# Optimization experiments

Measured on AMD Instinct MI355X. Metric: run time of the kernel, lower is better.

Reference implementation:

```python
import jax, jax.numpy as jnp
import numpy as np

N = 2000  # nodes per graph (hardcoded in the original module)


def gatv2(x, src, dst, edge_attr, Wl, Wr, We, att, b):
    """PyG GATv2Conv (concat=True, negative_slope=0.2, edge_dim) forward.
    x: [N, Fin]; src/dst: [E]; edge_attr: [E, 2]; att: [H, C]. Returns [N, H*C]."""
    n = x.shape[0]
    H, C = att.shape
    xl = (x @ Wl).reshape(n, H, C)            # messages from source nodes
    xr = (x @ Wr).reshape(n, H, C)            # target-node term
    ee = (edge_attr @ We).reshape(-1, H, C)   # edge feature term
    m = jax.nn.leaky_relu(xl[src] + xr[dst] + ee, 0.2)
    logits = jnp.einsum('ehc,hc->eh', m, att)           # [E, H]
    lmax = jax.ops.segment_max(logits, dst, num_segments=n)
    p = jnp.exp(logits - lmax[dst])
    denom = jax.ops.segment_sum(p, dst, num_segments=n)
    alpha = p / (denom[dst] + 1e-16)                    # scatter-softmax over in-edges
    out = jax.ops.segment_sum(alpha[:, :, None] * xl[src], dst, num_segments=n)
    return out.reshape(n, H * C) + b


def setup_inputs() -> dict:
    key = jax.random.key(0)
    ks = jax.random.split(key, 32)
    B, T, F, E = 4, 10, 8, 16000
    s = 0.05
    d = {
        'x': jax.random.normal(ks[0], (B, T, N, F), jnp.float32),
        'edge_index': jax.random.randint(ks[1], (2, E), 0, N, jnp.int32),
        'edge_attr': jax.random.normal(ks[2], (E, 2), jnp.float32),
        'w_l0': s * jax.random.normal(ks[3], (8, 128)),
        'w_r0': s * jax.random.normal(ks[4], (8, 128)),
        'w_e0': s * jax.random.normal(ks[5], (2, 128)),
        'att0': s * jax.random.normal(ks[6], (4, 32)),
        'b0': s * jax.random.normal(ks[7], (128,)),
        'w_l1': s * jax.random.normal(ks[8], (128, 128)),
        'w_r1': s * jax.random.normal(ks[9], (128, 128)),
        'w_e1': s * jax.random.normal(ks[10], (2, 128)),
        'att1': s * jax.random.normal(ks[11], (4, 32)),
        'b1': s * jax.random.normal(ks[12], (128,)),
        'w_l2': s * jax.random.normal(ks[13], (128, 32)),
        'w_r2': s * jax.random.normal(ks[14], (128, 32)),
        'w_e2': s * jax.random.normal(ks[15], (2, 32)),
        'att2': s * jax.random.normal(ks[16], (4, 8)),
        'b2': s * jax.random.normal(ks[17], (32,)),
        'w_ih': s * jax.random.normal(ks[18], (1024, 64000)),
        'w_hh': s * jax.random.normal(ks[19], (1024, 256)),
        'b_ih': s * jax.random.normal(ks[20], (1024,)),
        'b_hh': s * jax.random.normal(ks[21], (1024,)),
        'fc1_w': s * jax.random.normal(ks[22], (256, 512)),
        'fc1_b': s * jax.random.normal(ks[23], (512,)),
        'fc2_w': s * jax.random.normal(ks[24], (512, 1)),
        'fc2_b': s * jax.random.normal(ks[25], (1,)),
    }
    return d


def reference(x, edge_index, edge_attr, w_l0, w_r0, w_e0, att0, b0,
              w_l1, w_r1, w_e1, att1, b1, w_l2, w_r2, w_e2, att2, b2,
              w_ih, w_hh, b_ih, b_hh, fc1_w, fc1_b, fc2_w, fc2_b):
    B, T = x.shape[0], x.shape[1]
    # PyG GATv2Conv add_self_loops=True with fill_value='mean' for edge_attr
    loop = jnp.arange(N, dtype=edge_index.dtype)
    src = jnp.concatenate([edge_index[0], loop])
    dst = jnp.concatenate([edge_index[1], loop])
    ea = jnp.concatenate([edge_attr, jnp.broadcast_to(edge_attr.mean(0), (N, 2))], axis=0)

    def gat_stack(xt):  # [N, F] -> [N*32] flattened embedding
        h = jax.nn.relu(gatv2(xt, src, dst, ea, w_l0, w_r0, w_e0, att0, b0))
        h = jax.nn.relu(gatv2(h, src, dst, ea, w_l1, w_r1, w_e1, att1, b1))
        h = jax.nn.relu(gatv2(h, src, dst, ea, w_l2, w_r2, w_e2, att2, b2))
        return h.reshape(-1)

    emb = jax.vmap(jax.vmap(gat_stack))(x)  # [B, T, 64000]

    # single-layer LSTM (torch gate order: i, f, g, o)
    Hh = w_hh.shape[1]
    def step(carry, xt):
        h, c = carry
        g = xt @ w_ih.T + h @ w_hh.T + (b_ih + b_hh)
        i, f, gg, o = jnp.split(g, 4, axis=-1)
        c = jax.nn.sigmoid(f) * c + jax.nn.sigmoid(i) * jnp.tanh(gg)
        h = jax.nn.sigmoid(o) * jnp.tanh(c)
        return (h, c), h
    h0 = jnp.zeros((B, Hh), emb.dtype)
    (_, _), hs = jax.lax.scan(step, (h0, h0), jnp.swapaxes(emb, 0, 1))  # hs: [T, B, Hh]

    last = jax.nn.relu(hs[-1])                       # relu(lstm_out)[:, -1, :]
    hid = jax.nn.relu(last @ fc1_w + fc1_b)          # (dropout=0 -> identity)
    return hid @ fc2_w + fc2_b                       # [B, 1]
```

## Files before the change

### kernel.cpp

```cpp
#include <hip/hip_runtime.h>
#include <hip/hip_bf16.h>
#include <math.h>

typedef __hip_bfloat16 bf16;
typedef __attribute__((ext_vector_type(8))) short short8;
typedef __attribute__((ext_vector_type(4))) float f32x4;

#define NNODES 2000
#define NEDGE_IN 16000
#define NEDGE 18000
#define NGRAPH 40
#define GATES_KS 80

__device__ __forceinline__ float bf2f(bf16 v){ return __bfloat162float(v); }
__device__ __forceinline__ bf16 f2bf(float v){ return __float2bfloat16(v); }
__device__ __forceinline__ short bfbits(float v){ bf16 t = __float2bfloat16(v); return *reinterpret_cast<short*>(&t); }
__device__ __forceinline__ float blo(unsigned u){ return __uint_as_float(u<<16); }
__device__ __forceinline__ float bhi(unsigned u){ return __uint_as_float(u & 0xffff0000u); }

__global__ __launch_bounds__(256) void k_setup(const float* __restrict__ ea, float* __restrict__ mean_ea,
                        const float* __restrict__ whh, unsigned* __restrict__ whhT2,
                        const float* __restrict__ w1a, const float* __restrict__ w1b,
                        const float* __restrict__ w2a, const float* __restrict__ w2b,
                        bf16* __restrict__ b1a, bf16* __restrict__ b1b,
                        bf16* __restrict__ b2a, bf16* __restrict__ b2b,
                        int* __restrict__ cnt, int* __restrict__ cursor,
                        const float* __restrict__ X, const float* __restrict__ Wa,
                        const float* __restrict__ Wb,
                        bf16* __restrict__ Ya, bf16* __restrict__ Yb){
  __shared__ float smem[2048];
  int bb = blockIdx.x, tid = threadIdx.x;
  if (bb >= 689){
    int blk = bb - 689;
    for (int i = tid; i < 1024; i += 256){ smem[i] = Wa[i]; smem[1024+i] = Wb[i]; }
    __syncthreads();
    int j  = tid & 127;
    int rg = tid >> 7;
    size_t m0 = (size_t)blk*8 + (size_t)rg*4;
    const float* x0 = X + m0*8;
    float a0=0.f,a1=0.f,a2=0.f,a3=0.f, b0=0.f,b1=0.f,b2=0.f,b3=0.f;
    #pragma unroll
    for (int k=0;k<8;k++){
      float wa = smem[k*128 + j], wb = smem[1024 + k*128 + j];
      float x_0 = x0[k], x_1 = x0[8+k], x_2 = x0[16+k], x_3 = x0[24+k];
      a0 += x_0*wa; a1 += x_1*wa; a2 += x_2*wa; a3 += x_3*wa;
      b0 += x_0*wb; b1 += x_1*wb; b2 += x_2*wb; b3 += x_3*wb;
    }
    bf16* ya = Ya + m0*128 + j;
    bf16* yb = Yb + m0*128 + j;
    ya[0]=f2bf(a0); ya[128]=f2bf(a1); ya[256]=f2bf(a2); ya[384]=f2bf(a3);
    yb[0]=f2bf(b0); yb[128]=f2bf(b1); yb[256]=f2bf(b2); yb[384]=f2bf(b3);
  } else if (bb == 0){
    float* s0l = smem; float* s1l = smem + 256;
    float s0=0.f, s1=0.f;
    for (int e = tid; e < NEDGE_IN; e += 256){ s0 += ea[2*e]; s1 += ea[2*e+1]; }
    s0l[tid]=s0; s1l[tid]=s1; __syncthreads();
    for (int d=128; d>=1; d>>=1){
      if (tid < d){ s0l[tid]+=s0l[tid+d]; s1l[tid]+=s1l[tid+d]; }
      __syncthreads();
    }
    if (tid==0){ mean_ea[0]=s0l[0]/(float)NEDGE_IN; mean_ea[1]=s1l[0]/(float)NEDGE_IN; }
  } else if (bb < 513){
    int idx = (bb-1)*256 + tid;
    int j = idx >> 7, kp = idx & 127;
    unsigned ulo = (unsigned)(unsigned short)bfbits(whh[j*256 + 2*kp]);
    unsigned uhi = (unsigned)(unsigned short)bfbits(whh[j*256 + 2*kp + 1]);
    whhT2[kp*1024 + j] = (uhi<<16) | ulo;
  } else if (bb < 673){
    int idx = (bb-513)*256 + tid;
    const float* src; bf16* dst; int n, local;
    if (idx < 16384){ src=w1a; dst=b1a; n=128; local=idx; }
    else if (idx < 32768){ src=w1b; dst=b1b; n=128; local=idx-16384; }
    else if (idx < 36864){ src=w2a; dst=b2a; n=32; local=idx-32768; }
    else { src=w2b; dst=b2b; n=32; local=idx-36864; }
    int k = local / n, c = local % n;
    dst[c*128 + k] = f2bf(src[local]);
  } else {
    int idx = (bb-673)*256 + tid;
    if (idx < 2000) cnt[idx] = 0;
    else if (idx < 4000) cursor[idx-2000] = 0;
  }
}

__global__ void k_count(const int* __restrict__ ei, int* __restrict__ cnt){
  int e = blockIdx.x*256 + threadIdx.x;
  if (e >= NEDGE) return;
  int d = (e < NEDGE_IN) ? ei[NEDGE_IN + e] : (e - NEDGE_IN);
  atomicAdd(&cnt[d], 1);
}

__global__ void k_scan(const int* __restrict__ cnt, int* __restrict__ off){
  __shared__ int s[2048];
  int lane = threadIdx.x;
  for (int i = lane; i < 2048; i += 64) s[i] = (i < NNODES) ? cnt[i] : 0;
  __syncthreads();
  int base = lane*32, run = 0;
  for (int j=0;j<32;j++){ int t = s[base+j]; s[base+j] = run; run += t; }
  int x = run;
  for (int d=1; d<64; d<<=1){ int y = __shfl_up(x, d); if (lane >= d) x += y; }
  int chunkOff = x - run;
  for (int j=0;j<32;j++){ int idx = base+j; if (idx <= NNODES) off[idx] = chunkOff + s[idx]; }
}

__global__ void k_scatter(const int* __restrict__ ei, const int* __restrict__ off,
                          int* __restrict__ cursor, const float* __restrict__ ea,
                          const float* __restrict__ mean_ea,
                          int* __restrict__ csr_src, float2* __restrict__ eaP){
  int e = blockIdx.x*256 + threadIdx.x;
  if (e >= NEDGE) return;
  int d, sn; float2 a;
  if (e < NEDGE_IN){ sn = ei[e]; d = ei[NEDGE_IN+e]; a = ((const float2*)ea)[e]; }
  else { sn = e-NEDGE_IN; d = sn; a.x = mean_ea[0]; a.y = mean_ea[1]; }
  int p = off[d] + atomicAdd(&cursor[d], 1);
  csr_src[p] = sn;
  eaP[p] = a;
}

template<int N>
__global__ __launch_bounds__(256) void k_gemm_mf2(const bf16* __restrict__ A, const bf16* __restrict__ BTa,
                                                  const bf16* __restrict__ BTb,
                                                  bf16* __restrict__ Ya, bf16* __restrict__ Yb){
  const int NT = N/16;
  int lane = threadIdx.x & 63, wv = threadIdx.x >> 6;
  size_t m0 = (size_t)blockIdx.x*128 + (size_t)wv*32;
  int r = lane & 15, kg = lane >> 4;
  const f32x4 zero = {0.f,0.f,0.f,0.f};
  f32x4 acca[2][NT], accb[2][NT];
  #pragma unroll
  for (int s=0;s<2;s++)
    #pragma unroll
    for (int t=0;t<NT;t++){ acca[s][t] = zero; accb[s][t] = zero; }
  #pragma unroll
  for (int c=0;c<4;c++){
    short8 a0 = *(const short8*)(A + (m0 + r)*128 + c*32 + kg*8);
    short8 a1 = *(const short8*)(A + (m0 + 16 + r)*128 + c*32 + kg*8);
    #pragma unroll
    for (int t=0;t<NT;t++){
      short8 ba = *(const short8*)(BTa + (size_t)(t*16 + r)*128 + c*32 + kg*8);
      short8 bb = *(const short8*)(BTb + (size_t)(t*16 + r)*128 + c*32 + kg*8);
      acca[0][t] = __builtin_amdgcn_mfma_f32_16x16x32_bf16(a0, ba, acca[0][t], 0,0,0);
      acca[1][t] = __builtin_amdgcn_mfma_f32_16x16x32_bf16(a1, ba, acca[1][t], 0,0,0);
      accb[0][t] = __builtin_amdgcn_mfma_f32_16x16x32_bf16(a0, bb, accb[0][t], 0,0,0);
      accb[1][t] = __builtin_amdgcn_mfma_f32_16x16x32_bf16(a1, bb, accb[1][t], 0,0,0);
    }
  }
  #pragma unroll
  for (int s=0;s<2;s++)
    #pragma unroll
    for (int t=0;t<NT;t++){
      size_t row = m0 + s*16 + kg*4;
      int col = t*16 + r;
      #pragma unroll
      for (int i=0;i<4;i++){
        Ya[(row+i)*N + col] = f2bf(acca[s][t][i]);
        Yb[(row+i)*N + col] = f2bf(accb[s][t][i]);
      }
    }
}

__global__ __launch_bounds__(256) void k_edge_g(const bf16* __restrict__ XL, const bf16* __restrict__ XR,
                                                const float2* __restrict__ eaP, const int* __restrict__ off,
                                                const int* __restrict__ csr_src, const float* __restrict__ att,
                                                const float* __restrict__ We, const float* __restrict__ bias,
                                                bf16* __restrict__ Hout){
  int tid = threadIdx.x;
  int ln = tid & 63;
  int gq = tid >> 6;
  int n  = blockIdx.x;
  int c0 = 2*ln;
  float av0 = att[c0], av1 = att[c0+1];
  float w00 = We[c0], w01 = We[c0+1];
  float w10 = We[128+c0], w11 = We[128+c0+1];
  const unsigned* XLu = (const unsigned*)XL;
  const unsigned* XRu = (const unsigned*)XR;
  float xr0[10], xr1[10], srun[10], acc0[10], acc1[10];
  #pragma unroll
  for (int t=0;t<10;t++){
    int g = gq*10 + t;
    unsigned xu = XRu[((size_t)g*NNODES + n)*64 + ln];
    xr0[t] = blo(xu); xr1[t] = bhi(xu);
    srun[t]=0.f; acc0[t]=0.f; acc1[t]=0.f;
  }
  int p0 = off[n], p1 = off[n+1];
  for (int p = p0; p < p1; ++p){
    int u = csr_src[p];
    float2 e = eaP[p];
    float ed0 = fmaf(e.x, w00, e.y*w10);
    float ed1 = fmaf(e.x, w01, e.y*w11);
    unsigned xl[10];
    #pragma unroll
    for (int t=0;t<10;t++){
      int g = gq*10 + t;
      xl[t] = XLu[((size_t)g*NNODES + u)*64 + ln];
    }
    #pragma unroll
    for (int t=0;t<10;t++){
      float x0 = blo(xl[t]), x1 = bhi(xl[t]);
      float s0 = x0 + xr0[t] + ed0;
      float s1 = x1 + xr1[t] + ed1;
      float m0 = fmaxf(s0, 0.2f*s0);
      float m1 = fmaxf(s1, 0.2f*s1);
      float c = fmaf(m0, av0, m1*av1);
      #pragma unroll
      for (int d=8; d>=1; d>>=1) c += __shfl_xor(c, d);
      float pe = __expf(c);
      srun[t] += pe;
      acc0[t] = fmaf(pe, x0, acc0[t]);
      acc1[t] = fmaf(pe, x1, acc1[t]);
    }
  }
  #pragma unroll
  for (int t=0;t<10;t++){
    int g = gq*10 + t;
    float inv = 1.f/(srun[t] + 1e-16f);
    float o0 = fmaf(acc0[t], inv, bias[c0]);
    float o1 = fmaf(acc1[t], inv, bias[c0+1]);
    o0 = fmaxf(o0, 0.f); o1 = fmaxf(o1, 0.f);
    unsigned r0 = (unsigned)(unsigned short)bfbits(o0);
    unsigned r1 = (unsigned)(unsigned short)bfbits(o1);
    ((unsigned*)Hout)[((size_t)g*NNODES + n)*64 + ln] = (r1<<16) | r0;
  }
}

template<int H, int C>
__global__ __launch_bounds__(256) void k_edge(const bf16* __restrict__ XL, const bf16* __restrict__ XR,
                                              const float2* __restrict__ eaP, const int* __restrict__ off,
                                              const int* __restrict__ csr_src, const float* __restrict__ att,
                                              const float* __restrict__ We, const float* __restrict__ bias,
                                              bf16* __restrict__ Hout){
  const int HC = H*C;
  const int LPN = HC/2;
  const int NPW = 64/LPN;
  const int NPB = 4*NPW;
  int tid = threadIdx.x;
  int lane = tid & 63, wv = tid >> 6;
  int ln = lane % LPN;
  int n  = blockIdx.x*NPB + wv*NPW + lane/LPN;
  int g  = blockIdx.y;
  int c0 = 2*ln;
  size_t gbase = (size_t)g*NNODES*HC;
  const unsigned* XLu = (const unsigned*)(XL + gbase);
  unsigned xru = ((const unsigned*)(XR + gbase))[n*LPN + ln];
  float xr0 = blo(xru), xr1 = bhi(xru);
  float av0 = att[c0], av1 = att[c0+1];
  float w00 = We[c0], w01 = We[c0+1];
  float w10 = We[HC+c0], w11 = We[HC+c0+1];
  float srun = 0.f, acc0 = 0.f, acc1 = 0.f;
  int p0 = off[n], p1 = off[n+1];
  int p = p0;
  for (; p+2 <= p1; p += 2){
    int uA = csr_src[p], uB = csr_src[p+1];
    float2 eA = eaP[p], eB = eaP[p+1];
    unsigned xlA = XLu[uA*LPN + ln];
    unsigned xlB = XLu[uB*LPN + ln];
    float xa0 = blo(xlA), xa1 = bhi(xlA);
    float xb0 = blo(xlB), xb1 = bhi(xlB);
    float sa0 = xa0 + fmaf(eA.x,w00, fmaf(eA.y,w10, xr0));
    float sa1 = xa1 + fmaf(eA.x,w01, fmaf(eA.y,w11, xr1));
    float sb0 = xb0 + fmaf(eB.x,w00, fmaf(eB.y,w10, xr0));
    float sb1 = xb1 + fmaf(eB.x,w01, fmaf(eB.y,w11, xr1));
    float ma0 = fmaxf(sa0, 0.2f*sa0), ma1 = fmaxf(sa1, 0.2f*sa1);
    float mb0 = fmaxf(sb0, 0.2f*sb0), mb1 = fmaxf(sb1, 0.2f*sb1);
    float cA = fmaf(ma0,av0, ma1*av1);
    float cB = fmaf(mb0,av0, mb1*av1);
    #pragma unroll
    for (int d=C/4; d>=1; d>>=1){ cA += __shfl_xor(cA, d); cB += __shfl_xor(cB, d); }
    float peA = __expf(cA), peB = __expf(cB);
    srun += peA + peB;
    acc0 = fmaf(peA, xa0, fmaf(peB, xb0, acc0));
    acc1 = fmaf(peA, xa1, fmaf(peB, xb1, acc1));
  }
  if (p < p1){
    int uA = csr_src[p];
    float2 eA = eaP[p];
    unsigned xlA = XLu[uA*LPN + ln];
    float xa0 = blo(xlA), xa1 = bhi(xlA);
    float sa0 = xa0 + fmaf(eA.x,w00, fmaf(eA.y,w10, xr0));
    float sa1 = xa1 + fmaf(eA.x,w01, fmaf(eA.y,w11, xr1));
    float ma0 = fmaxf(sa0, 0.2f*sa0), ma1 = fmaxf(sa1, 0.2f*sa1);
    float cA = fmaf(ma0,av0, ma1*av1);
    #pragma unroll
    for (int d=C/4; d>=1; d>>=1) cA += __shfl_xor(cA, d);
    float peA = __expf(cA);
    srun += peA;
    acc0 = fmaf(peA, xa0, acc0);
    acc1 = fmaf(peA, xa1, acc1);
  }
  float inv = 1.f/(srun + 1e-16f);
  float o0 = fmaf(acc0, inv, bias[c0]);
  float o1 = fmaf(acc1, inv, bias[c0+1]);
  o0 = fmaxf(o0, 0.f); o1 = fmaxf(o1, 0.f);
  unsigned r0 = (unsigned)(unsigned short)bfbits(o0);
  unsigned r1 = (unsigned)(unsigned short)bfbits(o1);
  ((unsigned*)(Hout + gbase))[n*LPN + ln] = (r1<<16) | r0;
}

__global__ __launch_bounds__(256) void k_gates_mf(const bf16* __restrict__ emb, const float* __restrict__ wih,
                                                  float* __restrict__ part){
  const int nk = 2000/GATES_KS;
  int lane = threadIdx.x & 63, wv = threadIdx.x >> 6;
  int r = lane & 15, kg = lane >> 4;
  int j0 = (blockIdx.x*4 + wv)*16;
  int ks = blockIdx.y;
  int k0 = ks*nk*32;
  const f32x4 zero = {0.f,0.f,0.f,0.f};
  f32x4 acc0 = zero, acc1 = zero, acc2 = zero;
  const float* wrow = wih + (size_t)(j0 + r)*64000;
  const bf16*  e0p  = emb + (size_t)r*64000;
  const bf16*  e1p  = emb + (size_t)(16+r)*64000;
  const bf16*  e2p  = emb + (size_t)(32+r)*64000;
  #pragma unroll 2
  for (int s=0; s<nk; ++s){
    int k = k0 + s*32 + kg*8;
    float4 wa = *(const float4*)(wrow + k);
    float4 wb = *(const float4*)(wrow + k + 4);
    short8 bfr;
    bfr[0]=bfbits(wa.x); bfr[1]=bfbits(wa.y); bfr[2]=bfbits(wa.z); bfr[3]=bfbits(wa.w);
    bfr[4]=bfbits(wb.x); bfr[5]=bfbits(wb.y); bfr[6]=bfbits(wb.z); bfr[7]=bfbits(wb.w);
    short8 a0 = *(const short8*)(e0p + k);
    short8 a1 = *(const short8*)(e1p + k);
    short8 a2 = *(const short8*)(e2p + k);
    acc0 = __builtin_amdgcn_mfma_f32_16x16x32_bf16(a0, bfr, acc0, 0,0,0);
    acc1 = __builtin_amdgcn_mfma_f32_16x16x32_bf16(a1, bfr, acc1, 0,0,0);
    acc2 = __builtin_amdgcn_mfma_f32_16x16x32_bf16(a2, bfr, acc2, 0,0,0);
  }
  int col = j0 + r;
  float* prow = part + (size_t)ks*40960;
  #pragma unroll
  for (int i=0;i<4;i++){
    int row = kg*4 + i;
    prow[(size_t)row*1024 + col] = acc0[i];
    prow[(size_t)(row+16)*1024 + col] = acc1[i];
    if (row + 32 < 40) prow[(size_t)(row+32)*1024 + col] = acc2[i];
  }
}

__global__ __launch_bounds__(256) void k_gred(const float* __restrict__ part, float* __restrict__ gates){
  int idx = blockIdx.x*256 + threadIdx.x;
  float s = 0.f;
  #pragma unroll 8
  for (int ks=0; ks<GATES_KS; ks++) s += part[(size_t)ks*40960 + idx];
  gates[idx] = s;
}

__global__ __launch_bounds__(1024) void k_lstm10h(const float* __restrict__ gates, const unsigned* __restrict__ whhT2,
                                                  const float* __restrict__ bih, const float* __restrict__ bhh,
                                                  const float* __restrict__ fc1w, const float* __restrict__ fc1b,
                                                  const float* __restrict__ fc2w, const float* __restrict__ fc2b,
                                                  float* __restrict__ out){
  __shared__ float hs[256];
  __shared__ float g[1024];
  int b = blockIdx.x, j = threadIdx.x;
  float c_reg = 0.f;
  if (j < 256) hs[j] = 0.f;
  float bias = bih[j] + bhh[j];
  __syncthreads();
  for (int t=0;t<10;t++){
    float acc = gates[(size_t)(b*10+t)*1024 + j] + bias;
    #pragma unroll 16
    for (int kp=0;kp<128;kp++){
      unsigned u = whhT2[kp*1024 + j];
      float2 h2 = *(const float2*)&hs[2*kp];
      acc = fmaf(blo(u), h2.x, acc);
      acc = fmaf(bhi(u), h2.y, acc);
    }
    g[j] = acc;
    __syncthreads();
    if (j < 256){
      float i_ = g[j], f_ = g[j+256], gg = g[j+512], o_ = g[j+768];
      float si = 1.f/(1.f+__expf(-i_));
      float sf = 1.f/(1.f+__expf(-f_));
      float so = 1.f/(1.f+__expf(-o_));
      c_reg = sf*c_reg + si*tanhf(gg);
      hs[j] = so*tanhf(c_reg);
    }
    __syncthreads();
  }
  if (j < 512){
    float acc = fc1b[j];
    for (int k=0;k<256;k++){
      float l = fmaxf(hs[k], 0.f);
      acc = fmaf(l, fc1w[k*512 + j], acc);
    }
    float hid = fmaxf(acc, 0.f);
    g[j] = hid * fc2w[j];
  }
  __syncthreads();
  for (int d=256; d>=1; d>>=1){
    if (j < d) g[j] += g[j+d];
    __syncthreads();
  }
  if (j==0) out[b] = g[0] + fc2b[0];
}

extern "C" void kernel_launch(void* const* d_in, const int* in_sizes, int n_in,
                              void* d_out, int out_size, void* d_ws, size_t ws_size,
                              hipStream_t stream){
  const float* x    = (const float*)d_in[0];
  const int*   ei   = (const int*)  d_in[1];
  const float* ea   = (const float*)d_in[2];
  const float* wl0  = (const float*)d_in[3];
  const float* wr0  = (const float*)d_in[4];
  const float* we0  = (const float*)d_in[5];
  const float* att0 = (const float*)d_in[6];
  const float* b0   = (const float*)d_in[7];
  const float* wl1  = (const float*)d_in[8];
  const float* wr1  = (const float*)d_in[9];
  const float* we1  = (const float*)d_in[10];
  const float* att1 = (const float*)d_in[11];
  const float* b1   = (const float*)d_in[12];
  const float* wl2  = (const float*)d_in[13];
  const float* wr2  = (const float*)d_in[14];
  const float* we2  = (const float*)d_in[15];
  const float* att2 = (const float*)d_in[16];
  const float* b2   = (const float*)d_in[17];
  const float* wih  = (const float*)d_in[18];
  const float* whh  = (const float*)d_in[19];
  const float* bih  = (const float*)d_in[20];
  const float* bhh  = (const float*)d_in[21];
  const float* fc1w = (const float*)d_in[22];
  const float* fc1b = (const float*)d_in[23];
  const float* fc2w = (const float*)d_in[24];
  const float* fc2b = (const float*)d_in[25];
  float* out = (float*)d_out;

  char* base = (char*)d_ws; size_t cur = 0;
  auto alloc = [&](size_t bytes)->void*{
    cur = (cur + 255) & ~(size_t)255; void* p = base + cur; cur += bytes; return p;
  };
  float* mean_ea = (float*)alloc(8);
  int*   cnt     = (int*)  alloc((size_t)NNODES*4);
  int*   off     = (int*)  alloc((size_t)(NNODES+1)*4);
  int*   cursor  = (int*)  alloc((size_t)NNODES*4);
  int*   csr_src = (int*)  alloc((size_t)NEDGE*4);
  float2* eaP    = (float2*)alloc((size_t)NEDGE*8);
  bf16*  XL      = (bf16*) alloc((size_t)80000*128*2);
  bf16*  XR      = (bf16*) alloc((size_t)80000*128*2);
  bf16*  HBUF    = (bf16*) alloc((size_t)80000*128*2);
  float* part    = (float*)alloc((size_t)GATES_KS*40960*4);
  float* gates   = (float*)alloc((size_t)40*1024*4);
  unsigned* whhT2= (unsigned*)alloc((size_t)128*1024*4);
  bf16*  bt1a    = (bf16*) alloc((size_t)128*128*2);
  bf16*  bt1b    = (bf16*) alloc((size_t)128*128*2);
  bf16*  bt2a    = (bf16*) alloc((size_t)32*128*2);
  bf16*  bt2b    = (bf16*) alloc((size_t)32*128*2);

  k_setup <<<10689,256,0,stream>>>(ea, mean_ea, whh, whhT2, wl1, wr1, wl2, wr2,
                                   bt1a, bt1b, bt2a, bt2b, cnt, cursor,
                                   x, wl0, wr0, XL, XR);
  k_count   <<<(NEDGE+255)/256,256,0,stream>>>(ei, cnt);
  k_scan    <<<1,64,0,stream>>>(cnt, off);
  k_scatter <<<(NEDGE+255)/256,256,0,stream>>>(ei, off, cursor, ea, mean_ea, csr_src, eaP);

  k_edge_g  <<<NNODES,256,0,stream>>>(XL,XR,eaP,off,csr_src,att0,we0,b0,HBUF);

  k_gemm_mf2<128> <<<625,256,0,stream>>>(HBUF, bt1a, bt1b, XL, XR);
  k_edge_g  <<<NNODES,256,0,stream>>>(XL,XR,eaP,off,csr_src,att1,we1,b1,HBUF);

  k_gemm_mf2<32> <<<625,256,0,stream>>>(HBUF, bt2a, bt2b, XL, XR);
  k_edge<4,8> <<<dim3(125,40),256,0,stream>>>(XL,XR,eaP,off,csr_src,att2,we2,b2,HBUF);

  k_gates_mf<<<dim3(16,GATES_KS),256,0,stream>>>(HBUF, wih, part);
  k_gred    <<<160,256,0,stream>>>(part, gates);

  k_lstm10h<<<4,1024,0,stream>>>(gates, whhT2, bih, bhh, fc1w, fc1b, fc2w, fc2b, out);
}
```

Baseline: 419.1 us.

## Switch node features to node-major, graph-interleaved layout for coalesced gathers

Feature buffers change from graph-major [g][n][C] to node-major [n][g][C], so gathering a source node's features for several graphs reads one contiguous region. The edge kernels, the first-layer projection and the gate GEMM's embedding indexing are all updated to match. k_edge_g is also split across two grid rows with 5 graphs per wave instead of 10, which doubles the block count and lowers per-thread register arrays. The risk is that other kernels assume the old row order: the row-wise GEMM is indifferent to it, but the LSTM gate input ordering must stay consistent.

```diff
diff --git a/kernel.cpp b/kernel.cpp
--- a/kernel.cpp
+++ b/kernel.cpp
@@ -37,6 +37,7 @@
     int j  = tid & 127;
     int rg = tid >> 7;
     size_t m0 = (size_t)blk*8 + (size_t)rg*4;
+    int g = (int)(m0/NNODES), n = (int)(m0%NNODES);
     const float* x0 = X + m0*8;
     float a0=0.f,a1=0.f,a2=0.f,a3=0.f, b0=0.f,b1=0.f,b2=0.f,b3=0.f;
     #pragma unroll
@@ -46,10 +47,11 @@
       a0 += x_0*wa; a1 += x_1*wa; a2 += x_2*wa; a3 += x_3*wa;
       b0 += x_0*wb; b1 += x_1*wb; b2 += x_2*wb; b3 += x_3*wb;
     }
-    bf16* ya = Ya + m0*128 + j;
-    bf16* yb = Yb + m0*128 + j;
-    ya[0]=f2bf(a0); ya[128]=f2bf(a1); ya[256]=f2bf(a2); ya[384]=f2bf(a3);
-    yb[0]=f2bf(b0); yb[128]=f2bf(b1); yb[256]=f2bf(b2); yb[384]=f2bf(b3);
+    const size_t RS = (size_t)NGRAPH*128;
+    bf16* ya = Ya + ((size_t)n*NGRAPH + g)*128 + j;
+    bf16* yb = Yb + ((size_t)n*NGRAPH + g)*128 + j;
+    ya[0]=f2bf(a0); ya[RS]=f2bf(a1); ya[2*RS]=f2bf(a2); ya[3*RS]=f2bf(a3);
+    yb[0]=f2bf(b0); yb[RS]=f2bf(b1); yb[2*RS]=f2bf(b2); yb[3*RS]=f2bf(b3);
   } else if (bb == 0){
     float* s0l = smem; float* s1l = smem + 256;
     float s0=0.f, s1=0.f;
@@ -167,17 +169,17 @@
   int ln = tid & 63;
   int gq = tid >> 6;
   int n  = blockIdx.x;
+  int g0 = blockIdx.y*20 + gq*5;
   int c0 = 2*ln;
   float av0 = att[c0], av1 = att[c0+1];
   float w00 = We[c0], w01 = We[c0+1];
   float w10 = We[128+c0], w11 = We[128+c0+1];
   const unsigned* XLu = (const unsigned*)XL;
   const unsigned* XRu = (const unsigned*)XR;
-  float xr0[10], xr1[10], srun[10], acc0[10], acc1[10];
-  #pragma unroll
-  for (int t=0;t<10;t++){
-    int g = gq*10 + t;
-    unsigned xu = XRu[((size_t)g*NNODES + n)*64 + ln];
+  float xr0[5], xr1[5], srun[5], acc0[5], acc1[5];
+  #pragma unroll
+  for (int t=0;t<5;t++){
+    unsigned xu = XRu[((size_t)n*NGRAPH + g0+t)*64 + ln];
     xr0[t] = blo(xu); xr1[t] = bhi(xu);
     srun[t]=0.f; acc0[t]=0.f; acc1[t]=0.f;
   }
@@ -187,14 +189,12 @@
     float2 e = eaP[p];
     float ed0 = fmaf(e.x, w00, e.y*w10);
     float ed1 = fmaf(e.x, w01, e.y*w11);
-    unsigned xl[10];
-    #pragma unroll
-    for (int t=0;t<10;t++){
-      int g = gq*10 + t;
-      xl[t] = XLu[((size_t)g*NNODES + u)*64 + ln];
-    }
-    #pragma unroll
-    for (int t=0;t<10;t++){
+    unsigned xl[5];
+    #pragma unroll
+    for (int t=0;t<5;t++)
+      xl[t] = XLu[((size_t)u*NGRAPH + g0+t)*64 + ln];
+    #pragma unroll
+    for (int t=0;t<5;t++){
       float x0 = blo(xl[t]), x1 = bhi(xl[t]);
       float s0 = x0 + xr0[t] + ed0;
       float s1 = x1 + xr1[t] + ed1;
@@ -210,15 +210,14 @@
     }
   }
   #pragma unroll
-  for (int t=0;t<10;t++){
-    int g = gq*10 + t;
+  for (int t=0;t<5;t++){
     float inv = 1.f/(srun[t] + 1e-16f);
     float o0 = fmaf(acc0[t], inv, bias[c0]);
     float o1 = fmaf(acc1[t], inv, bias[c0+1]);
     o0 = fmaxf(o0, 0.f); o1 = fmaxf(o1, 0.f);
     unsigned r0 = (unsigned)(unsigned short)bfbits(o0);
     unsigned r1 = (unsigned)(unsigned short)bfbits(o1);
-    ((unsigned*)Hout)[((size_t)g*NNODES + n)*64 + ln] = (r1<<16) | r0;
+    ((unsigned*)Hout)[((size_t)n*NGRAPH + g0+t)*64 + ln] = (r1<<16) | r0;
   }
 }
 
@@ -238,9 +237,8 @@
   int n  = blockIdx.x*NPB + wv*NPW + lane/LPN;
   int g  = blockIdx.y;
   int c0 = 2*ln;
-  size_t gbase = (size_t)g*NNODES*HC;
-  const unsigned* XLu = (const unsigned*)(XL + gbase);
-  unsigned xru = ((const unsigned*)(XR + gbase))[n*LPN + ln];
+  const unsigned* XLu = (const unsigned*)XL;
+  unsigned xru = ((const unsigned*)XR)[((size_t)n*NGRAPH + g)*LPN + ln];
   float xr0 = blo(xru), xr1 = bhi(xru);
   float av0 = att[c0], av1 = att[c0+1];
   float w00 = We[c0], w01 = We[c0+1];
@@ -251,8 +249,8 @@
   for (; p+2 <= p1; p += 2){
     int uA = csr_src[p], uB = csr_src[p+1];
     float2 eA = eaP[p], eB = eaP[p+1];
-    unsigned xlA = XLu[uA*LPN + ln];
-    unsigned xlB = XLu[uB*LPN + ln];
+    unsigned xlA = XLu[((size_t)uA*NGRAPH + g)*LPN + ln];
+    unsigned xlB = XLu[((size_t)uB*NGRAPH + g)*LPN + ln];
     float xa0 = blo(xlA), xa1 = bhi(xlA);
     float xb0 = blo(xlB), xb1 = bhi(xlB);
     float sa0 = xa0 + fmaf(eA.x,w00, fmaf(eA.y,w10, xr0));
@@ -273,7 +271,7 @@
   if (p < p1){
     int uA = csr_src[p];
     float2 eA = eaP[p];
-    unsigned xlA = XLu[uA*LPN + ln];
+    unsigned xlA = XLu[((size_t)uA*NGRAPH + g)*LPN + ln];
     float xa0 = blo(xlA), xa1 = bhi(xlA);
     float sa0 = xa0 + fmaf(eA.x,w00, fmaf(eA.y,w10, xr0));
     float sa1 = xa1 + fmaf(eA.x,w01, fmaf(eA.y,w11, xr1));
@@ -292,7 +290,7 @@
   o0 = fmaxf(o0, 0.f); o1 = fmaxf(o1, 0.f);
   unsigned r0 = (unsigned)(unsigned short)bfbits(o0);
   unsigned r1 = (unsigned)(unsigned short)bfbits(o1);
-  ((unsigned*)(Hout + gbase))[n*LPN + ln] = (r1<<16) | r0;
+  ((unsigned*)Hout)[((size_t)n*NGRAPH + g)*LPN + ln] = (r1<<16) | r0;
 }
 
 __global__ __launch_bounds__(256) void k_gates_mf(const bf16* __restrict__ emb, const float* __restrict__ wih,
@@ -306,20 +304,21 @@
   const f32x4 zero = {0.f,0.f,0.f,0.f};
   f32x4 acc0 = zero, acc1 = zero, acc2 = zero;
   const float* wrow = wih + (size_t)(j0 + r)*64000;
-  const bf16*  e0p  = emb + (size_t)r*64000;
-  const bf16*  e1p  = emb + (size_t)(16+r)*64000;
-  const bf16*  e2p  = emb + (size_t)(32+r)*64000;
+  const bf16* e0p = emb + (size_t)r*32 + kg*8;
+  const bf16* e1p = emb + (size_t)(16+r)*32 + kg*8;
+  const bf16* e2p = emb + (size_t)(32+r)*32 + kg*8;
   #pragma unroll 2
   for (int s=0; s<nk; ++s){
     int k = k0 + s*32 + kg*8;
+    size_t aoff = (size_t)((k0>>5) + s)*(NGRAPH*32);
     float4 wa = *(const float4*)(wrow + k);
     float4 wb = *(const float4*)(wrow + k + 4);
     short8 bfr;
     bfr[0]=bfbits(wa.x); bfr[1]=bfbits(wa.y); bfr[2]=bfbits(wa.z); bfr[3]=bfbits(wa.w);
     bfr[4]=bfbits(wb.x); bfr[5]=bfbits(wb.y); bfr[6]=bfbits(wb.z); bfr[7]=bfbits(wb.w);
-    short8 a0 = *(const short8*)(e0p + k);
-    short8 a1 = *(const short8*)(e1p + k);
-    short8 a2 = *(const short8*)(e2p + k);
+    short8 a0 = *(const short8*)(e0p + aoff);
+    short8 a1 = *(const short8*)(e1p + aoff);
+    short8 a2 = *(const short8*)(e2p + aoff);
     acc0 = __builtin_amdgcn_mfma_f32_16x16x32_bf16(a0, bfr, acc0, 0,0,0);
     acc1 = __builtin_amdgcn_mfma_f32_16x16x32_bf16(a1, bfr, acc1, 0,0,0);
     acc2 = __builtin_amdgcn_mfma_f32_16x16x32_bf16(a2, bfr, acc2, 0,0,0);
@@ -452,10 +451,10 @@
   k_scan    <<<1,64,0,stream>>>(cnt, off);
   k_scatter <<<(NEDGE+255)/256,256,0,stream>>>(ei, off, cursor, ea, mean_ea, csr_src, eaP);
 
-  k_edge_g  <<<NNODES,256,0,stream>>>(XL,XR,eaP,off,csr_src,att0,we0,b0,HBUF);
+  k_edge_g  <<<dim3(NNODES,2),256,0,stream>>>(XL,XR,eaP,off,csr_src,att0,we0,b0,HBUF);
 
   k_gemm_mf2<128> <<<625,256,0,stream>>>(HBUF, bt1a, bt1b, XL, XR);
-  k_edge_g  <<<NNODES,256,0,stream>>>(XL,XR,eaP,off,csr_src,att1,we1,b1,HBUF);
+  k_edge_g  <<<dim3(NNODES,2),256,0,stream>>>(XL,XR,eaP,off,csr_src,att1,we1,b1,HBUF);
 
   k_gemm_mf2<32> <<<625,256,0,stream>>>(HBUF, bt2a, bt2b, XL, XR);
   k_edge<4,8> <<<dim3(125,40),256,0,stream>>>(XL,XR,eaP,off,csr_src,att2,we2,b2,HBUF);
```

Result: faster. 370.2 us (-11.7%).
